# Kernel optimization log

Measured on AMD Instinct MI355X. Metric: run time of the kernel, lower is better.

The kernel has to match this reference:

```python
import jax, jax.numpy as jnp
import numpy as np

N, B, D, Q = 32, 36, 2048, 1024  # batch, objects, v_dim, q_dim


def setup_inputs() -> dict:
    key = jax.random.key(0)
    ks = jax.random.split(key, 6)
    sc = 0.02  # small init so ReLU chains stay well-scaled
    return {
        "v": jax.random.normal(ks[0], (N, B, D), jnp.float32),
        "q": jax.random.normal(ks[1], (N, Q), jnp.float32),
        "W1": jax.random.normal(ks[2], (D, D), jnp.float32) * sc,
        "b1": jnp.zeros((D,), jnp.float32),
        "W2": jax.random.normal(ks[3], (D, D), jnp.float32) * sc,
        "b2": jnp.zeros((D,), jnp.float32),
        "W3": jax.random.normal(ks[4], (Q, D), jnp.float32) * sc,
        "b3": jnp.zeros((D,), jnp.float32),
    }


def reference(v, q, W1, b1, W2, b2, W3, b3):
    # FCNet = ReLU(Linear(.)) with weight-norm folded, dropout=0 (eval).
    # Original calls linear3 twice (linear4 unused bug), so q_emb == q_emb2.
    qe = jax.nn.relu(q @ W3 + b3)  # (N, D)
    # pairs[n,i,j] = v[n,i]*qe[n] + v[n,j]*qe[n]  -> (N, B, B, D)
    pairs = (v[:, :, None, :] + v[:, None, :, :]) * qe[:, None, None, :]
    h = jax.nn.relu(jnp.einsum('nijd,de->nije', pairs, W1) + b1)  # linear1
    x = jnp.sum(h, axis=2)  # sum over j relations -> (N, B, D)
    return jax.nn.relu(x @ W2 + b2)  # linear2
```

## Files before the change

### kernel.cpp

```cpp
#include <hip/hip_runtime.h>
#include <stdint.h>

#define N_BATCH 32
#define B_OBJ   36
#define D_DIM   2048
#define Q_DIM   1024

typedef __bf16 bf16x8 __attribute__((ext_vector_type(8)));
typedef float  f32x4  __attribute__((ext_vector_type(4)));

__device__ __forceinline__ uint16_t f2bf(float f) {
    uint32_t u = __builtin_bit_cast(uint32_t, f);
    uint32_t r = (u + 0x7FFFu + ((u >> 16) & 1u)) >> 16;
    return (uint16_t)r;
}

__device__ __forceinline__ void gld_lds16(const void* g, void* l) {
    __builtin_amdgcn_global_load_lds(
        (const __attribute__((address_space(1))) uint32_t*)g,
        (__attribute__((address_space(3))) uint32_t*)l, 16, 0, 0);
}

__global__ __launch_bounds__(256) void transpose_all(
    const float* __restrict__ W1, const float* __restrict__ W2,
    const float* __restrict__ W3,
    uint16_t* __restrict__ W1t, uint16_t* __restrict__ W2t,
    uint16_t* __restrict__ W3t) {
    __shared__ float tile[64][65];
    int gy = blockIdx.y;
    const float* W; uint16_t* Wt; int K, k0;
    if (gy < 32)      { W = W1; Wt = W1t; K = 2048; k0 = gy * 64; }
    else if (gy < 64) { W = W2; Wt = W2t; K = 2048; k0 = (gy - 32) * 64; }
    else              { W = W3; Wt = W3t; K = 1024; k0 = (gy - 64) * 64; }
    int n0 = blockIdx.x * 64;
    int t = threadIdx.x;
    {
        int r = t >> 4, c = (t & 15) * 4;
#pragma unroll
        for (int p = 0; p < 4; ++p)
            *(float4*)&tile[r + p * 16][c] =
                *(const float4*)&W[(size_t)(k0 + r + p * 16) * 2048 + n0 + c];
    }
    __syncthreads();
    {
        int n = t >> 2, kb = (t & 3) * 16;
#pragma unroll
        for (int g4 = 0; g4 < 4; ++g4) {
            int k = kb + g4 * 4;
            ushort4 o;
            o.x = f2bf(tile[k][n]);     o.y = f2bf(tile[k + 1][n]);
            o.z = f2bf(tile[k + 2][n]); o.w = f2bf(tile[k + 3][n]);
            *(ushort4*)&Wt[(size_t)(n0 + n) * K + k0 + k] = o;
        }
    }
}

__global__ __launch_bounds__(256) void qk_gemm(
    const float* __restrict__ q,
    const uint16_t* __restrict__ W3t,
    float* __restrict__ qpart) {
    __shared__ __align__(16) uint16_t As[32][32];
    __shared__ __align__(16) uint16_t Bs[128][32];
    int t = threadIdx.x, lane = t & 63, wave = t >> 6;
    int l15 = lane & 15, quad = lane >> 4;
    int n0 = blockIdx.x * 128;
    int kbase = blockIdx.y * 256;
    f32x4 acc[2][2] = {};
    int ar = t >> 3, ac = (t & 7) * 4;
    int br = t >> 2, bk = (t & 3) * 8;

    for (int k0 = 0; k0 < 256; k0 += 32) {
        __syncthreads();
        float4 av = *(const float4*)&q[(size_t)ar * Q_DIM + kbase + k0 + ac];
        ushort4 a4;
        a4.x = f2bf(av.x); a4.y = f2bf(av.y); a4.z = f2bf(av.z); a4.w = f2bf(av.w);
        *(ushort4*)&As[ar][ac] = a4;
        *(uint4*)&Bs[br][bk]      = *(const uint4*)&W3t[(size_t)(n0 + br) * Q_DIM + kbase + k0 + bk];
        *(uint4*)&Bs[br + 64][bk] = *(const uint4*)&W3t[(size_t)(n0 + br + 64) * Q_DIM + kbase + k0 + bk];
        __syncthreads();
        bf16x8 af[2], bfr[2];
        af[0]  = *(const bf16x8*)&As[l15][quad * 8];
        af[1]  = *(const bf16x8*)&As[16 + l15][quad * 8];
        bfr[0] = *(const bf16x8*)&Bs[wave * 32 + l15][quad * 8];
        bfr[1] = *(const bf16x8*)&Bs[wave * 32 + 16 + l15][quad * 8];
#pragma unroll
        for (int i = 0; i < 2; ++i)
#pragma unroll
            for (int j = 0; j < 2; ++j)
                acc[i][j] = __builtin_amdgcn_mfma_f32_16x16x32_bf16(af[i], bfr[j], acc[i][j], 0, 0, 0);
    }
    float* dst = qpart + (size_t)blockIdx.y * 32 * D_DIM;
#pragma unroll
    for (int i = 0; i < 2; ++i)
#pragma unroll
        for (int j = 0; j < 2; ++j) {
            int n = n0 + wave * 32 + j * 16 + l15;
#pragma unroll
            for (int r = 0; r < 4; ++r)
                dst[(size_t)(i * 16 + quad * 4 + r) * D_DIM + n] = acc[i][j][r];
        }
}

__global__ void qe_reduce(const float* __restrict__ qpart,
                          const float* __restrict__ b3,
                          float* __restrict__ qe) {
    int i = blockIdx.x * 256 + threadIdx.x;
    const float4* p = (const float4*)qpart;
    float4 s = p[i];
    float4 s1 = p[16384 + i], s2 = p[32768 + i], s3 = p[49152 + i];
    float4 b = ((const float4*)b3)[i & 511];
    float4 o;
    o.x = fmaxf(s.x + s1.x + s2.x + s3.x + b.x, 0.f);
    o.y = fmaxf(s.y + s1.y + s2.y + s3.y + b.y, 0.f);
    o.z = fmaxf(s.z + s1.z + s2.z + s3.z + b.z, 0.f);
    o.w = fmaxf(s.w + s1.w + s2.w + s3.w + b.w, 0.f);
    ((float4*)qe)[i] = o;
}

__global__ void make_u(const float* __restrict__ v,
                       const float* __restrict__ qe,
                       uint16_t* __restrict__ u) {
    int idx = blockIdx.x * 256 + threadIdx.x;
    const int total = (N_BATCH * B_OBJ * D_DIM) / 4;
    if (idx >= total) return;
    int d4 = idx % (D_DIM / 4);
    int nb = idx / ((B_OBJ * D_DIM) / 4);
    float4 vv = ((const float4*)v)[idx];
    float4 qq = ((const float4*)qe)[(size_t)nb * (D_DIM / 4) + d4];
    ushort4 o;
    o.x = f2bf(vv.x * qq.x);
    o.y = f2bf(vv.y * qq.y);
    o.z = f2bf(vv.z * qq.z);
    o.w = f2bf(vv.w * qq.w);
    ((ushort4*)u)[idx] = o;
}

__global__ __launch_bounds__(256) void gemm_batch(
    const uint16_t* __restrict__ A,
    const uint16_t* __restrict__ Bt,
    const float* __restrict__ bias,
    void* __restrict__ Cv,
    int mode) {
    __shared__ __align__(16) uint16_t smem[2][11264];
    float* yt = (float*)&smem[0][0];

    int t = threadIdx.x, lane = t & 63, wave = t >> 6;
    int l15 = lane & 15, quad = lane >> 4;
    int nb = blockIdx.y;
    int n0 = blockIdx.x * 128;
    const uint16_t* Ab = A + (size_t)nb * B_OBJ * D_DIM;

    const uint16_t* gp[6];
    int loff[6];
    int wslot = (lane & 3) ^ ((lane >> 2) & 3);
#pragma unroll
    for (int c = 0; c < 6; ++c) {
        int r = wave + 4 * c;
        int rr = (r < 22) ? r : 0;
        if (rr < 6) {
            int h = rr / 3, g = rr % 3;
            int row = g * 16 + (lane >> 2), kk = h * 32 + wslot * 8;
            gp[c] = Ab + (size_t)row * D_DIM + kk;
            loff[c] = h * 1536 + g * 512;
        } else {
            int rb = rr - 6, h = rb >> 3, g = rb & 7;
            int row = g * 16 + (lane >> 2), kk = h * 32 + wslot * 8;
            gp[c] = Bt + (size_t)(n0 + row) * D_DIM + kk;
            loff[c] = 3072 + h * 4096 + g * 512;
        }
    }

    f32x4 acc[3][2] = {};

#pragma unroll
    for (int c = 0; c < 6; ++c)
        if (wave + 4 * c < 22) gld_lds16(gp[c], &smem[0][loff[c]]);
    __syncthreads();

    int rslot = quad ^ (l15 & 3);

    int buf = 0;
    for (int k0 = 0; k0 < D_DIM; k0 += 64) {
        int nk = k0 + 64;
        if (nk < D_DIM) {
#pragma unroll
            for (int c = 0; c < 6; ++c)
                if (wave + 4 * c < 22) gld_lds16(gp[c] + nk, &smem[buf ^ 1][loff[c]]);
        }
        const uint16_t* As = &smem[buf][0];
        const uint16_t* Bs = As + 3072;
#pragma unroll
        for (int s = 0; s < 2; ++s) {
            bf16x8 af[3], bfr[2];
#pragma unroll
            for (int i = 0; i < 3; ++i)
                af[i] = *(const bf16x8*)(As + s * 1536 + (i * 16 + l15) * 32 + rslot * 8);
#pragma unroll
            for (int j = 0; j < 2; ++j)
                bfr[j] = *(const bf16x8*)(Bs + s * 4096 + (wave * 32 + j * 16 + l15) * 32 + rslot * 8);
#pragma unroll
            for (int i = 0; i < 3; ++i)
#pragma unroll
                for (int j = 0; j < 2; ++j)
                    acc[i][j] = __builtin_amdgcn_mfma_f32_16x16x32_bf16(af[i], bfr[j], acc[i][j], 0, 0, 0);
        }
        __syncthreads();
        buf ^= 1;
    }

    if (mode == 0) {
        uint16_t* X = (uint16_t*)Cv;
#pragma unroll
        for (int i = 0; i < 3; ++i)
#pragma unroll
            for (int j = 0; j < 2; ++j)
#pragma unroll
                for (int r = 0; r < 4; ++r)
                    yt[(i * 16 + quad * 4 + r) * 132 + wave * 32 + j * 16 + l15] = acc[i][j][r];
        __syncthreads();
        int col = t & 127, half = t >> 7;
        float b = bias[n0 + col];
        float z[36];
#pragma unroll
        for (int j = 0; j < 36; ++j) z[j] = yt[j * 132 + col];
#pragma unroll
        for (int ii = 0; ii < 18; ++ii) {
            int i = half * 18 + ii;
            float zi = z[i] + b;
            float s = 0.f;
#pragma unroll
            for (int j = 0; j < 36; ++j) s += fmaxf(zi + z[j], 0.f);
            X[(size_t)(nb * B_OBJ + i) * D_DIM + n0 + col] = f2bf(s);
        }
    } else {
        float* O = (float*)Cv;
#pragma unroll
        for (int i = 0; i < 3; ++i)
#pragma unroll
            for (int r = 0; r < 4; ++r) {
                int row = i * 16 + quad * 4 + r;
                if (row < B_OBJ) {
#pragma unroll
                    for (int j = 0; j < 2; ++j) {
                        int cc = n0 + wave * 32 + j * 16 + l15;
                        O[(size_t)(nb * B_OBJ + row) * D_DIM + cc] =
                            fmaxf(acc[i][j][r] + bias[cc], 0.f);
                    }
                }
            }
    }
}

extern "C" void kernel_launch(void* const* d_in, const int* in_sizes, int n_in,
                              void* d_out, int out_size, void* d_ws, size_t ws_size,
                              hipStream_t stream) {
    const float* v  = (const float*)d_in[0];
    const float* q  = (const float*)d_in[1];
    const float* W1 = (const float*)d_in[2];
    const float* b1 = (const float*)d_in[3];
    const float* W2 = (const float*)d_in[4];
    const float* b2 = (const float*)d_in[5];
    const float* W3 = (const float*)d_in[6];
    const float* b3 = (const float*)d_in[7];
    float* out = (float*)d_out;

    char* ws = (char*)d_ws;
    uint16_t* W1t   = (uint16_t*)(ws + 0);
    uint16_t* W2t   = (uint16_t*)(ws + 8388608);
    uint16_t* W3t   = (uint16_t*)(ws + 16777216);
    uint16_t* u     = (uint16_t*)(ws + 16777216);
    float*    qpart = (float*)   (ws + 21495808);
    float*    qe    = (float*)   (ws + 22544384);
    uint16_t* x     = (uint16_t*)(ws + 22806528);

    transpose_all<<<dim3(32, 80), 256, 0, stream>>>(W1, W2, W3, W1t, W2t, W3t);

    qk_gemm<<<dim3(16, 4), 256, 0, stream>>>(q, W3t, qpart);
    qe_reduce<<<64, 256, 0, stream>>>(qpart, b3, qe);

    make_u<<<(N_BATCH * B_OBJ * D_DIM / 4 + 255) / 256, 256, 0, stream>>>(v, qe, u);

    gemm_batch<<<dim3(16, N_BATCH), 256, 0, stream>>>(u, W1t, b1, x, 0);

    gemm_batch<<<dim3(16, N_BATCH), 256, 0, stream>>>(x, W2t, b2, out, 1);
}
```

Measured before the change: 178.8 us.

## Prefetch two K-stages ahead with counted vmcnt waits and padded A tile

Changes the GEMM main loop from a one-stage-ahead double buffer guarded by full __syncthreads to a scheme where two stages are in flight. Each wait uses an explicit s_waitcnt vmcnt(6), so only the older stage must land before the barrier. The A tile is padded from 48 to 64 rows so every wave issues exactly 6 uniform loads, which removes the per-load predicate and keeps the vmcnt accounting exact. The cost is extra wasted load bandwidth and LDS for the padded rows, plus an extra barrier per iteration.

```diff
diff --git a/kernel.cpp b/kernel.cpp
--- a/kernel.cpp
+++ b/kernel.cpp
@@ -141,7 +141,7 @@
     const float* __restrict__ bias,
     void* __restrict__ Cv,
     int mode) {
-    __shared__ __align__(16) uint16_t smem[2][11264];
+    __shared__ __align__(16) uint16_t smem[2][12288];
     float* yt = (float*)&smem[0][0];
 
     int t = threadIdx.x, lane = t & 63, wave = t >> 6;
@@ -156,45 +156,44 @@
 #pragma unroll
     for (int c = 0; c < 6; ++c) {
         int r = wave + 4 * c;
-        int rr = (r < 22) ? r : 0;
-        if (rr < 6) {
-            int h = rr / 3, g = rr % 3;
+        if (r < 8) {
+            int h = r >> 2, g = r & 3;
             int row = g * 16 + (lane >> 2), kk = h * 32 + wslot * 8;
             gp[c] = Ab + (size_t)row * D_DIM + kk;
-            loff[c] = h * 1536 + g * 512;
+            loff[c] = h * 2048 + g * 512;
         } else {
-            int rb = rr - 6, h = rb >> 3, g = rb & 7;
+            int rb = r - 8, h = rb >> 3, g = rb & 7;
             int row = g * 16 + (lane >> 2), kk = h * 32 + wslot * 8;
             gp[c] = Bt + (size_t)(n0 + row) * D_DIM + kk;
-            loff[c] = 3072 + h * 4096 + g * 512;
+            loff[c] = 4096 + h * 4096 + g * 512;
         }
     }
 
     f32x4 acc[3][2] = {};
-
-#pragma unroll
-    for (int c = 0; c < 6; ++c)
-        if (wave + 4 * c < 22) gld_lds16(gp[c], &smem[0][loff[c]]);
-    __syncthreads();
-
     int rslot = quad ^ (l15 & 3);
 
-    int buf = 0;
-    for (int k0 = 0; k0 < D_DIM; k0 += 64) {
-        int nk = k0 + 64;
-        if (nk < D_DIM) {
-#pragma unroll
-            for (int c = 0; c < 6; ++c)
-                if (wave + 4 * c < 22) gld_lds16(gp[c] + nk, &smem[buf ^ 1][loff[c]]);
-        }
-        const uint16_t* As = &smem[buf][0];
-        const uint16_t* Bs = As + 3072;
+#define STAGE(kk, bi)                                   \
+    {                                                   \
+        _Pragma("unroll")                               \
+        for (int c = 0; c < 6; ++c)                     \
+            gld_lds16(gp[c] + (kk), &smem[bi][loff[c]]); \
+    }
+
+    STAGE(0, 0);
+    STAGE(64, 1);
+    asm volatile("s_waitcnt vmcnt(6)" ::: "memory");
+    __builtin_amdgcn_s_barrier();
+
+    int cur = 0;
+    for (int k = 0; k < 32; ++k) {
+        const uint16_t* As = &smem[cur][0];
+        const uint16_t* Bs = As + 4096;
 #pragma unroll
         for (int s = 0; s < 2; ++s) {
             bf16x8 af[3], bfr[2];
 #pragma unroll
             for (int i = 0; i < 3; ++i)
-                af[i] = *(const bf16x8*)(As + s * 1536 + (i * 16 + l15) * 32 + rslot * 8);
+                af[i] = *(const bf16x8*)(As + s * 2048 + (i * 16 + l15) * 32 + rslot * 8);
 #pragma unroll
             for (int j = 0; j < 2; ++j)
                 bfr[j] = *(const bf16x8*)(Bs + s * 4096 + (wave * 32 + j * 16 + l15) * 32 + rslot * 8);
@@ -204,12 +203,22 @@
                 for (int j = 0; j < 2; ++j)
                     acc[i][j] = __builtin_amdgcn_mfma_f32_16x16x32_bf16(af[i], bfr[j], acc[i][j], 0, 0, 0);
         }
-        __syncthreads();
-        buf ^= 1;
-    }
+        if (k == 31) break;
+        __builtin_amdgcn_s_barrier();
+        if (k + 2 < 32) {
+            STAGE((k + 2) * 64, cur);
+            asm volatile("s_waitcnt vmcnt(6)" ::: "memory");
+        } else {
+            asm volatile("s_waitcnt vmcnt(0)" ::: "memory");
+        }
+        __builtin_amdgcn_s_barrier();
+        cur ^= 1;
+    }
+#undef STAGE
 
     if (mode == 0) {
         uint16_t* X = (uint16_t*)Cv;
+        __syncthreads();
 #pragma unroll
         for (int i = 0; i < 3; ++i)
 #pragma unroll
```

Result: faster. 174.5 us (-2.4%).

## Triple-buffer GEMM LDS pipeline and fuse qe reduction into make_u

Applied to the files above, without the earlier changes.

The batched GEMM moves from double-buffered to triple-buffered LDS staging in dynamic shared memory. Explicit vmcnt waits and raw barriers keep two loads in flight ahead of compute. Separately, qe_reduce and make_u become one kernel: each thread computes its qe slice once and loops over the 36 objects, which drops a launch and the qe round-trip. The risks are lower occupancy from the larger LDS footprint, hand-counted vmcnt values that must match the per-wave load counts, and a small fused grid of 128 blocks with a serial loop.

```diff
diff --git a/kernel.cpp b/kernel.cpp
--- a/kernel.cpp
+++ b/kernel.cpp
@@ -101,38 +101,33 @@
         }
 }
 
-__global__ void qe_reduce(const float* __restrict__ qpart,
-                          const float* __restrict__ b3,
-                          float* __restrict__ qe) {
-    int i = blockIdx.x * 256 + threadIdx.x;
+__global__ __launch_bounds__(128) void qe_make_u(
+    const float* __restrict__ qpart, const float* __restrict__ b3,
+    const float* __restrict__ v, uint16_t* __restrict__ u) {
+    int nb = blockIdx.y;
+    int d4 = blockIdx.x * 128 + threadIdx.x;
     const float4* p = (const float4*)qpart;
-    float4 s = p[i];
-    float4 s1 = p[16384 + i], s2 = p[32768 + i], s3 = p[49152 + i];
-    float4 b = ((const float4*)b3)[i & 511];
-    float4 o;
-    o.x = fmaxf(s.x + s1.x + s2.x + s3.x + b.x, 0.f);
-    o.y = fmaxf(s.y + s1.y + s2.y + s3.y + b.y, 0.f);
-    o.z = fmaxf(s.z + s1.z + s2.z + s3.z + b.z, 0.f);
-    o.w = fmaxf(s.w + s1.w + s2.w + s3.w + b.w, 0.f);
-    ((float4*)qe)[i] = o;
-}
-
-__global__ void make_u(const float* __restrict__ v,
-                       const float* __restrict__ qe,
-                       uint16_t* __restrict__ u) {
-    int idx = blockIdx.x * 256 + threadIdx.x;
-    const int total = (N_BATCH * B_OBJ * D_DIM) / 4;
-    if (idx >= total) return;
-    int d4 = idx % (D_DIM / 4);
-    int nb = idx / ((B_OBJ * D_DIM) / 4);
-    float4 vv = ((const float4*)v)[idx];
-    float4 qq = ((const float4*)qe)[(size_t)nb * (D_DIM / 4) + d4];
-    ushort4 o;
-    o.x = f2bf(vv.x * qq.x);
-    o.y = f2bf(vv.y * qq.y);
-    o.z = f2bf(vv.z * qq.z);
-    o.w = f2bf(vv.w * qq.w);
-    ((ushort4*)u)[idx] = o;
+    size_t base = (size_t)nb * 512 + d4;
+    float4 s0 = p[base], s1 = p[16384 + base], s2 = p[32768 + base], s3 = p[49152 + base];
+    float4 b = ((const float4*)b3)[d4];
+    float4 qe;
+    qe.x = fmaxf(s0.x + s1.x + s2.x + s3.x + b.x, 0.f);
+    qe.y = fmaxf(s0.y + s1.y + s2.y + s3.y + b.y, 0.f);
+    qe.z = fmaxf(s0.z + s1.z + s2.z + s3.z + b.z, 0.f);
+    qe.w = fmaxf(s0.w + s1.w + s2.w + s3.w + b.w, 0.f);
+    const float4* v4 = (const float4*)v;
+    ushort4* u4 = (ushort4*)u;
+    size_t rb = (size_t)nb * B_OBJ * 512 + d4;
+#pragma unroll 4
+    for (int i = 0; i < B_OBJ; ++i) {
+        float4 vv = v4[rb + (size_t)i * 512];
+        ushort4 o;
+        o.x = f2bf(vv.x * qe.x);
+        o.y = f2bf(vv.y * qe.y);
+        o.z = f2bf(vv.z * qe.z);
+        o.w = f2bf(vv.w * qe.w);
+        u4[rb + (size_t)i * 512] = o;
+    }
 }
 
 __global__ __launch_bounds__(256) void gemm_batch(
@@ -141,8 +136,8 @@
     const float* __restrict__ bias,
     void* __restrict__ Cv,
     int mode) {
-    __shared__ __align__(16) uint16_t smem[2][11264];
-    float* yt = (float*)&smem[0][0];
+    extern __shared__ __align__(16) uint16_t smem[];
+    float* yt = (float*)smem;
 
     int t = threadIdx.x, lane = t & 63, wave = t >> 6;
     int l15 = lane & 15, quad = lane >> 4;
@@ -171,23 +166,27 @@
     }
 
     f32x4 acc[3][2] = {};
-
-#pragma unroll
-    for (int c = 0; c < 6; ++c)
-        if (wave + 4 * c < 22) gld_lds16(gp[c], &smem[0][loff[c]]);
-    __syncthreads();
-
     int rslot = quad ^ (l15 & 3);
-
-    int buf = 0;
-    for (int k0 = 0; k0 < D_DIM; k0 += 64) {
-        int nk = k0 + 64;
-        if (nk < D_DIM) {
-#pragma unroll
-            for (int c = 0; c < 6; ++c)
-                if (wave + 4 * c < 22) gld_lds16(gp[c] + nk, &smem[buf ^ 1][loff[c]]);
-        }
-        const uint16_t* As = &smem[buf][0];
+    bool w01 = (wave < 2);
+
+#define STAGE(kk, bi)                                                    \
+    {                                                                    \
+        _Pragma("unroll")                                                \
+        for (int c = 0; c < 6; ++c)                                      \
+            if (wave + 4 * c < 22)                                       \
+                gld_lds16(gp[c] + (kk), smem + (bi) * 11264 + loff[c]);  \
+    }
+
+    STAGE(0, 0);
+    STAGE(64, 1);
+    STAGE(128, 2);
+    if (w01) asm volatile("s_waitcnt vmcnt(12)" ::: "memory");
+    else     asm volatile("s_waitcnt vmcnt(10)" ::: "memory");
+    __builtin_amdgcn_s_barrier();
+
+    int cur = 0;
+    for (int k = 0; k < 32; ++k) {
+        const uint16_t* As = smem + cur * 11264;
         const uint16_t* Bs = As + 3072;
 #pragma unroll
         for (int s = 0; s < 2; ++s) {
@@ -204,12 +203,26 @@
                 for (int j = 0; j < 2; ++j)
                     acc[i][j] = __builtin_amdgcn_mfma_f32_16x16x32_bf16(af[i], bfr[j], acc[i][j], 0, 0, 0);
         }
-        __syncthreads();
-        buf ^= 1;
-    }
+        if (k == 31) break;
+        __builtin_amdgcn_s_barrier();
+        if (k <= 28) {
+            STAGE((k + 3) * 64, cur);
+            if (w01) asm volatile("s_waitcnt vmcnt(12)" ::: "memory");
+            else     asm volatile("s_waitcnt vmcnt(10)" ::: "memory");
+        } else if (k == 29) {
+            if (w01) asm volatile("s_waitcnt vmcnt(6)" ::: "memory");
+            else     asm volatile("s_waitcnt vmcnt(5)" ::: "memory");
+        } else {
+            asm volatile("s_waitcnt vmcnt(0)" ::: "memory");
+        }
+        __builtin_amdgcn_s_barrier();
+        cur = (cur == 2) ? 0 : cur + 1;
+    }
+#undef STAGE
 
     if (mode == 0) {
         uint16_t* X = (uint16_t*)Cv;
+        __syncthreads();
 #pragma unroll
         for (int i = 0; i < 3; ++i)
 #pragma unroll
@@ -270,17 +283,22 @@
     uint16_t* W3t   = (uint16_t*)(ws + 16777216);
     uint16_t* u     = (uint16_t*)(ws + 16777216);
     float*    qpart = (float*)   (ws + 21495808);
-    float*    qe    = (float*)   (ws + 22544384);
     uint16_t* x     = (uint16_t*)(ws + 22806528);
 
+    static bool attr_done = false;
+    if (!attr_done) {
+        (void)hipFuncSetAttribute((const void*)gemm_batch,
+                                  hipFuncAttributeMaxDynamicSharedMemorySize, 67584);
+        attr_done = true;
+    }
+
     transpose_all<<<dim3(32, 80), 256, 0, stream>>>(W1, W2, W3, W1t, W2t, W3t);
 
     qk_gemm<<<dim3(16, 4), 256, 0, stream>>>(q, W3t, qpart);
-    qe_reduce<<<64, 256, 0, stream>>>(qpart, b3, qe);
-
-    make_u<<<(N_BATCH * B_OBJ * D_DIM / 4 + 255) / 256, 256, 0, stream>>>(v, qe, u);
-
-    gemm_batch<<<dim3(16, N_BATCH), 256, 0, stream>>>(u, W1t, b1, x, 0);
-
-    gemm_batch<<<dim3(16, N_BATCH), 256, 0, stream>>>(x, W2t, b2, out, 1);
-}
+
+    qe_make_u<<<dim3(4, N_BATCH), 128, 0, stream>>>(qpart, b3, v, u);
+
+    gemm_batch<<<dim3(16, N_BATCH), 256, 67584, stream>>>(u, W1t, b1, x, 0);
+
+    gemm_batch<<<dim3(16, N_BATCH), 256, 67584, stream>>>(x, W2t, b2, out, 1);
+}
```

Result: no change. 176.3 us (-1.4%).
